# Optimization experiments

Hardware: AMD Instinct MI355X
Metric: run time of the kernel (lower is better)

Reference implementation:

```python
import jax, jax.numpy as jnp
import numpy as np

B = 16      # batch (num jagged sequences)
N = 1024    # max seq length (mask size n)
D = 512     # embedding_dim
H = 8       # num_heads
DA = 64     # attention_dim per head
DV = 64     # linear_hidden_dim per head
EPS = 1e-6


def setup_inputs() -> dict:
    key = jax.random.key(0)
    k0, k1, k2, k3 = jax.random.split(key, 4)
    lengths = 512 + 16 * np.arange(B)            # deterministic jagged lengths, all <= N
    offsets = np.concatenate([[0], np.cumsum(lengths)]).astype(np.int64)  # (B+1,)
    T = int(offsets[-1])                          # 10112 total tokens
    x = jax.random.normal(k0, (T, D), jnp.float32)
    uvqk = jax.random.normal(k1, (D, 2 * H * DV + 2 * H * DA), jnp.float32) * 0.02
    # torch Linear weight is (out_features, in_features) = (D, H*DV), xavier-uniform scale
    lim = float(np.sqrt(6.0 / (D + H * DV)))
    o_weight = jax.random.uniform(k2, (D, H * DV), jnp.float32, -lim, lim)
    o_bias = jax.random.uniform(k3, (D,), jnp.float32, -0.01, 0.01)
    invalid_attn_mask = jnp.tril(jnp.ones((N, N), jnp.float32))  # causal {0,1} mask
    return {
        "x": x,
        "x_offsets": jnp.asarray(offsets),
        "invalid_attn_mask": invalid_attn_mask,
        "uvqk": uvqk,
        "o_weight": o_weight,
        "o_bias": o_bias,
    }


def _layer_norm(x):
    # F.layer_norm over last dim, no elementwise affine
    m = jnp.mean(x, axis=-1, keepdims=True)
    v = jnp.mean(jnp.square(x - m), axis=-1, keepdims=True)
    return (x - m) / jnp.sqrt(v + EPS)


def _jagged_to_padded(values, offsets, n):
    # values: (T, C) -> (B, n, C), zero padded
    lengths = offsets[1:] - offsets[:-1]               # (B,)
    pos = jnp.arange(n)                                # (n,)
    idx = offsets[:-1, None] + pos[None, :]            # (B, n)
    valid = pos[None, :] < lengths[:, None]            # (B, n)
    idx = jnp.where(valid, idx, 0)
    return values[idx] * valid[..., None].astype(values.dtype)


def _dense_to_jagged(padded, offsets, T):
    # padded: (B, n, C) -> (T, C)
    tok = jnp.arange(T)
    b = jnp.searchsorted(offsets, tok, side="right") - 1   # batch id per token
    p = tok - offsets[b]                                   # position within sequence
    return padded[b, p]


def reference(x, x_offsets, invalid_attn_mask, uvqk, o_weight, o_bias):
    T = x.shape[0]
    n = invalid_attn_mask.shape[-1]
    normed_x = _layer_norm(x)                              # (T, D)
    mm = jax.nn.silu(normed_x @ uvqk)                      # (T, 2*H*DV + 2*H*DA)
    u, v, q, k = jnp.split(mm, [H * DV, 2 * H * DV, 2 * H * DV + H * DA], axis=1)
    pq = _jagged_to_padded(q, x_offsets, n).reshape(-1, n, H, DA)  # (B,n,H,DA)
    pk = _jagged_to_padded(k, x_offsets, n).reshape(-1, n, H, DA)
    pv = _jagged_to_padded(v, x_offsets, n).reshape(-1, n, H, DV)
    qk = jnp.einsum("bqhd,bkhd->bhqk", pq, pk)             # (B,H,n,n)
    qk = (jax.nn.silu(qk) / n) * invalid_attn_mask[None, None]
    attn = jnp.einsum("bhqk,bkhd->bqhd", qk, pv).reshape(-1, n, H * DV)
    attn_j = _dense_to_jagged(attn, x_offsets, T)          # (T, H*DV)
    o_input = u * _layer_norm(attn_j)
    return o_input @ o_weight.T + o_bias + x
```

## Files before the change

### kernel.cpp

```cpp
#include <hip/hip_runtime.h>
#include <hip/hip_bf16.h>
#include <math.h>

typedef short bf16x8 __attribute__((ext_vector_type(8)));
typedef float f32x4 __attribute__((ext_vector_type(4)));

#define MFMA16x16(a, b, c) __builtin_amdgcn_mfma_f32_16x16x32_bf16(a, b, c, 0, 0, 0)

__device__ __forceinline__ float silu_f(float v) { return v / (1.0f + __expf(-v)); }
__device__ __forceinline__ int swz128(int b) { return b ^ (((b >> 7) & 7) << 4); }

__device__ __forceinline__ unsigned short f2bf(float f) {
  union { float f; unsigned u; } x; x.f = f;
  unsigned r = x.u + 0x7fffu + ((x.u >> 16) & 1u);
  return (unsigned short)(r >> 16);
}
__device__ __forceinline__ float bf2f(unsigned short h) {
  union { unsigned u; float f; } x; x.u = ((unsigned)h) << 16;
  return x.f;
}

__device__ __forceinline__ void gload_lds16(const void* g, void* l) {
  __builtin_amdgcn_global_load_lds((__attribute__((address_space(1))) unsigned int*)g,
                                   (__attribute__((address_space(3))) unsigned int*)l,
                                   16, 0, 0);
}

__global__ void k_prep_offs(const int* __restrict__ raw, int* __restrict__ offs, int Bp1) {
  int t = threadIdx.x;
  bool is64 = (raw[3] == 0);
  if (t < Bp1) offs[t] = is64 ? raw[2 * t] : raw[t];
}

__global__ __launch_bounds__(256) void k_conv_uvqkT(const float* __restrict__ uvqk,
                                                    unsigned short* __restrict__ uvqkT) {
  __shared__ float tile[32][33];
  int n0 = blockIdx.x * 32, k0 = blockIdx.y * 32;
  int tx = threadIdx.x & 31;
  int ty = threadIdx.x >> 5;
#pragma unroll
  for (int i = 0; i < 4; ++i)
    tile[ty + 8 * i][tx] = uvqk[(size_t)(k0 + ty + 8 * i) * 2048 + n0 + tx];
  __syncthreads();
#pragma unroll
  for (int i = 0; i < 4; ++i) {
    int nn = ty + 8 * i;
    uvqkT[(size_t)(n0 + nn) * 512 + k0 + tx] = f2bf(tile[tx][nn]);
  }
}

__global__ __launch_bounds__(256) void k_conv_bf16(const float* __restrict__ in,
                                                   unsigned short* __restrict__ out, int n) {
  int i = blockIdx.x * 256 + threadIdx.x;
  if (i < n) out[i] = f2bf(in[i]);
}

__global__ __launch_bounds__(256) void k_ln_x(const float* __restrict__ x,
                                              unsigned short* __restrict__ normed, int T) {
  int lane = threadIdx.x & 63, wid = threadIdx.x >> 6;
  int row = blockIdx.x * 4 + wid;
  if (row >= T) return;
  const float4* xr = (const float4*)(x + (size_t)row * 512);
  float4 a = xr[lane * 2], b = xr[lane * 2 + 1];
  float s = a.x + a.y + a.z + a.w + b.x + b.y + b.z + b.w;
  float s2 = a.x * a.x + a.y * a.y + a.z * a.z + a.w * a.w +
             b.x * b.x + b.y * b.y + b.z * b.z + b.w * b.w;
#pragma unroll
  for (int m = 1; m < 64; m <<= 1) { s += __shfl_xor(s, m); s2 += __shfl_xor(s2, m); }
  float mean = s * (1.0f / 512.0f);
  float var = s2 * (1.0f / 512.0f) - mean * mean;
  float rstd = rsqrtf(var + 1e-6f);
  float v[8] = {a.x, a.y, a.z, a.w, b.x, b.y, b.z, b.w};
  unsigned short o[8];
#pragma unroll
  for (int j = 0; j < 8; ++j) o[j] = f2bf((v[j] - mean) * rstd);
  *(uint4*)(normed + (size_t)row * 512 + lane * 8) = *(uint4*)o;
}

__global__ __launch_bounds__(256) void k_ln_mul_u(const unsigned short* __restrict__ attnb,
                                                  const unsigned short* __restrict__ mm,
                                                  unsigned short* __restrict__ oin, int T) {
  int lane = threadIdx.x & 63, wid = threadIdx.x >> 6;
  int row = blockIdx.x * 4 + wid;
  if (row >= T) return;
  uint4 av = *(const uint4*)(attnb + (size_t)row * 512 + lane * 8);
  const unsigned short* ae = (const unsigned short*)&av;
  float v[8];
#pragma unroll
  for (int j = 0; j < 8; ++j) v[j] = bf2f(ae[j]);
  float s = 0.f, s2 = 0.f;
#pragma unroll
  for (int j = 0; j < 8; ++j) { s += v[j]; s2 += v[j] * v[j]; }
#pragma unroll
  for (int m = 1; m < 64; m <<= 1) { s += __shfl_xor(s, m); s2 += __shfl_xor(s2, m); }
  float mean = s * (1.0f / 512.0f);
  float var = s2 * (1.0f / 512.0f) - mean * mean;
  float rstd = rsqrtf(var + 1e-6f);
  uint4 ub = *(const uint4*)(mm + (size_t)row * 2048 + lane * 8);
  const unsigned short* us = (const unsigned short*)&ub;
  unsigned short o[8];
#pragma unroll
  for (int j = 0; j < 8; ++j) o[j] = f2bf((v[j] - mean) * rstd * bf2f(us[j]));
  *(uint4*)(oin + (size_t)row * 512 + lane * 8) = *(uint4*)o;
}

template <int MODE>
__global__ __launch_bounds__(256) void k_gemm_bt(const unsigned short* __restrict__ A,
                                                 const unsigned short* __restrict__ Bt,
                                                 void* __restrict__ Cout,
                                                 const float* __restrict__ bias,
                                                 const float* __restrict__ xres,
                                                 int M, int Nn, int K, int ntn) {
  __shared__ __align__(16) char lds[32768];
  char* ldsA = lds;
  char* ldsB = lds + 16384;
  int bid = blockIdx.x;
  int mt = bid / ntn, nt = bid - mt * ntn;
  int m0 = mt * 128, n0 = nt * 128;
  int tid = threadIdx.x, lane = tid & 63, wid = tid >> 6;
  int wm = wid >> 1, wn = wid & 1;
  int fr = lane & 15, fq = lane >> 4;
  f32x4 acc[4][4] = {};
  int nK = K >> 6;
  int lco = (lane & 7) * 16;
  int lrow8 = lane >> 3;
  for (int kt = 0; kt < nK; ++kt) {
    int k0 = kt << 6;
#pragma unroll
    for (int p = 0; p < 4; ++p) {
      int chunk = wid * 4 + p;
      int row = chunk * 8 + lrow8;
      int colb = lco ^ ((row & 7) << 4);
      int ar = m0 + row; if (ar >= M) ar = M - 1;
      gload_lds16((const char*)(A + (size_t)ar * K + k0) + colb, ldsA + chunk * 1024);
      gload_lds16((const char*)(Bt + (size_t)(n0 + row) * K + k0) + colb, ldsB + chunk * 1024);
    }
    __syncthreads();
    bf16x8 af[4][2], bfr[4][2];
#pragma unroll
    for (int mi = 0; mi < 4; ++mi) {
      int r = wm * 64 + mi * 16 + fr;
#pragma unroll
      for (int kk = 0; kk < 2; ++kk)
        af[mi][kk] = *(const bf16x8*)(ldsA + swz128(r * 128 + kk * 64 + fq * 16));
    }
#pragma unroll
    for (int ni = 0; ni < 4; ++ni) {
      int r = wn * 64 + ni * 16 + fr;
#pragma unroll
      for (int kk = 0; kk < 2; ++kk)
        bfr[ni][kk] = *(const bf16x8*)(ldsB + swz128(r * 128 + kk * 64 + fq * 16));
    }
#pragma unroll
    for (int mi = 0; mi < 4; ++mi)
#pragma unroll
      for (int ni = 0; ni < 4; ++ni) {
        acc[mi][ni] = MFMA16x16(af[mi][0], bfr[ni][0], acc[mi][ni]);
        acc[mi][ni] = MFMA16x16(af[mi][1], bfr[ni][1], acc[mi][ni]);
      }
    __syncthreads();
  }
#pragma unroll
  for (int mi = 0; mi < 4; ++mi) {
#pragma unroll
    for (int j = 0; j < 4; ++j) {
      int r = m0 + wm * 64 + mi * 16 + fq * 4 + j;
      if (r >= M) continue;
#pragma unroll
      for (int ni = 0; ni < 4; ++ni) {
        int c = n0 + wn * 64 + ni * 16 + fr;
        float v = acc[mi][ni][j];
        if (MODE == 0) {
          ((unsigned short*)Cout)[(size_t)r * Nn + c] = f2bf(silu_f(v));
        } else {
          ((float*)Cout)[(size_t)r * Nn + c] = v + bias[c] + xres[(size_t)r * 512 + c];
        }
      }
    }
  }
}

__global__ __launch_bounds__(256) void k_vT(const unsigned short* __restrict__ mm,
                                            const int* __restrict__ offs,
                                            unsigned short* __restrict__ vT) {
  int bh = blockIdx.x; int b = bh >> 3, h = bh & 7;
  int off = offs[b], len = offs[b + 1] - off;
  int lane = threadIdx.x & 63, w = threadIdx.x >> 6;
  const unsigned short* vp = mm + (size_t)off * 2048 + 512 + h * 64 + lane;
  unsigned short* vt = vT + ((size_t)bh * 64 + lane) * 1024;
  int nc = ((len + 63) & ~63) >> 3;
  for (int c = w; c < nc; c += 4) {
    int s8 = c << 3;
    unsigned short r[8];
#pragma unroll
    for (int j = 0; j < 8; ++j)
      r[j] = (s8 + j < len) ? vp[(size_t)(s8 + j) * 2048] : (unsigned short)0;
    *(uint4*)(vt + s8) = *(uint4*)r;
  }
}

__global__ __launch_bounds__(256) void k_attn2(const unsigned short* __restrict__ mm,
                                               const unsigned short* __restrict__ vT,
                                               const int* __restrict__ offs,
                                               unsigned short* __restrict__ attnb,
                                               float inv_n) {
  __shared__ __align__(16) char sP[16384];
  int bid = blockIdx.x;
  int orig = (bid & 7) * 128 + (bid >> 3);
  int bh = orig >> 3, grp = orig & 7;
  int b = bh >> 3, h = bh & 7;
  int off = offs[b], len = offs[b + 1] - off;
  int tid = threadIdx.x, lane = tid & 63, wid = tid >> 6;
  int qb = grp * 128 + wid * 32;
  if (qb >= len) return;
  int fr = lane & 15, fq = lane >> 4;
  const unsigned short* qp = mm + (size_t)off * 2048 + 1024 + h * 64;
  const unsigned short* kp = mm + (size_t)off * 2048 + 1536 + h * 64;
  const unsigned short* vtp = vT + (size_t)bh * 64 * 1024;
  bf16x8 aq[2][2];
#pragma unroll
  for (int mi = 0; mi < 2; ++mi) {
    int qr = qb + mi * 16 + fr; if (qr >= len) qr = len - 1;
#pragma unroll
    for (int kk = 0; kk < 2; ++kk)
      aq[mi][kk] = *(const bf16x8*)(qp + (size_t)qr * 2048 + kk * 32 + fq * 8);
  }
  f32x4 accO[2][4] = {};
  char* pw = sP + wid * 4096;
  int nkt = (qb >> 6) + 1;
  for (int kt = 0; kt < nkt; ++kt) {
    int s0 = kt << 6;
    bf16x8 kf[4][2];
#pragma unroll
    for (int ni = 0; ni < 4; ++ni)
#pragma unroll
      for (int kk = 0; kk < 2; ++kk)
        kf[ni][kk] = *(const bf16x8*)(kp + (size_t)(s0 + ni * 16 + fr) * 2048 + kk * 32 + fq * 8);
#pragma unroll
    for (int mi = 0; mi < 2; ++mi) {
      f32x4 sacc[4] = {};
#pragma unroll
      for (int ni = 0; ni < 4; ++ni) {
        sacc[ni] = MFMA16x16(aq[mi][0], kf[ni][0], sacc[ni]);
        sacc[ni] = MFMA16x16(aq[mi][1], kf[ni][1], sacc[ni]);
      }
#pragma unroll
      for (int ni = 0; ni < 4; ++ni)
#pragma unroll
        for (int j = 0; j < 4; ++j) {
          int pq = qb + mi * 16 + fq * 4 + j;
          int ps = s0 + ni * 16 + fr;
          float v = (ps <= pq) ? silu_f(sacc[ni][j]) * inv_n : 0.0f;
          *(unsigned short*)(pw + swz128((mi * 16 + fq * 4 + j) * 128 + (ni * 16 + fr) * 2)) =
              f2bf(v);
        }
    }
    bf16x8 vf[4][2];
#pragma unroll
    for (int nd = 0; nd < 4; ++nd)
#pragma unroll
      for (int kk = 0; kk < 2; ++kk)
        vf[nd][kk] = *(const bf16x8*)(vtp + (size_t)(nd * 16 + fr) * 1024 + s0 + kk * 32 + fq * 8);
#pragma unroll
    for (int mi = 0; mi < 2; ++mi) {
      bf16x8 pa0 = *(const bf16x8*)(pw + swz128((mi * 16 + fr) * 128 + fq * 16));
      bf16x8 pa1 = *(const bf16x8*)(pw + swz128((mi * 16 + fr) * 128 + 64 + fq * 16));
#pragma unroll
      for (int nd = 0; nd < 4; ++nd) {
        accO[mi][nd] = MFMA16x16(pa0, vf[nd][0], accO[mi][nd]);
        accO[mi][nd] = MFMA16x16(pa1, vf[nd][1], accO[mi][nd]);
      }
    }
  }
#pragma unroll
  for (int mi = 0; mi < 2; ++mi)
#pragma unroll
    for (int nd = 0; nd < 4; ++nd)
#pragma unroll
      for (int j = 0; j < 4; ++j) {
        int pq = qb + mi * 16 + fq * 4 + j;
        if (pq < len)
          attnb[(size_t)(off + pq) * 512 + h * 64 + nd * 16 + fr] = f2bf(accO[mi][nd][j]);
      }
}

extern "C" void kernel_launch(void* const* d_in, const int* in_sizes, int n_in,
                              void* d_out, int out_size, void* d_ws, size_t ws_size,
                              hipStream_t stream) {
  const float* x = (const float*)d_in[0];
  const int* xoff = (const int*)d_in[1];
  const float* uvqk = (const float*)d_in[3];
  const float* ow = (const float*)d_in[4];
  const float* obias = (const float*)d_in[5];

  const int D = 512;
  int T = in_sizes[0] / D;
  int B = in_sizes[1] - 1;
  int nm = 1;
  while ((long long)nm * nm < (long long)in_sizes[2]) nm <<= 1;

  char* w = (char*)d_ws;
  size_t p = 0;
  auto alloc = [&](size_t bytes) { size_t r = p; p += (bytes + 255) & ~(size_t)255; return r; };
  int* offs = (int*)(w + alloc(sizeof(int) * (size_t)(B + 1)));
  unsigned short* normed = (unsigned short*)(w + alloc((size_t)T * 512 * 2));
  unsigned short* mm = (unsigned short*)(w + alloc((size_t)T * 2048 * 2));
  unsigned short* attnb = (unsigned short*)(w + alloc((size_t)T * 512 * 2));
  unsigned short* oin = (unsigned short*)(w + alloc((size_t)T * 512 * 2));
  unsigned short* uvqkT = (unsigned short*)(w + alloc((size_t)2048 * 512 * 2));
  unsigned short* owb = (unsigned short*)(w + alloc((size_t)512 * 512 * 2));
  unsigned short* vT = (unsigned short*)(w + alloc((size_t)B * 8 * 64 * (size_t)nm * 2));

  k_prep_offs<<<1, 32, 0, stream>>>(xoff, offs, B + 1);
  k_conv_uvqkT<<<dim3(64, 16), 256, 0, stream>>>(uvqk, uvqkT);
  k_conv_bf16<<<1024, 256, 0, stream>>>(ow, owb, 512 * 512);
  k_ln_x<<<(T + 3) / 4, 256, 0, stream>>>(x, normed, T);
  int ntm = (T + 127) / 128;
  k_gemm_bt<0><<<ntm * 16, 256, 0, stream>>>(normed, uvqkT, (void*)mm, nullptr, nullptr,
                                             T, 2048, 512, 16);
  k_vT<<<B * 8, 256, 0, stream>>>(mm, offs, vT);
  k_attn2<<<(B * 8 * nm / 128), 256, 0, stream>>>(mm, vT, offs, attnb, 1.0f / (float)nm);
  k_ln_mul_u<<<(T + 3) / 4, 256, 0, stream>>>(attnb, mm, oin, T);
  k_gemm_bt<1><<<ntm * 4, 256, 0, stream>>>(oin, owb, d_out, obias, x, T, 512, 512, 4);
}
```

Measured before the change: 261.8 us.

## Schedule attention work by descending q-tile with compacted K buffer

A prep kernel builds a list of valid (batch, q-tile) work items ordered from longest causal range to shortest, and the attention kernel assigns one wave per (tile, head) from that list. Waves for q-tiles past the sequence end are no longer launched, and long tiles start first to balance the load. K is also copied into a contiguous per-head buffer so its loads are dense rather than strided by 2048, and the QK loop is restructured to reuse each K fragment across both M sub-tiles. The cost is an extra K copy pass, a serial single-thread tile build, and more workspace.

```diff
diff --git a/kernel.cpp b/kernel.cpp
--- a/kernel.cpp
+++ b/kernel.cpp
@@ -26,10 +26,23 @@
                                    16, 0, 0);
 }
 
-__global__ void k_prep_offs(const int* __restrict__ raw, int* __restrict__ offs, int Bp1) {
+__global__ void k_prep(const int* __restrict__ raw, int Bp1, int* __restrict__ offs,
+                       int* __restrict__ tiles, int qtmax) {
   int t = threadIdx.x;
   bool is64 = (raw[3] == 0);
   if (t < Bp1) offs[t] = is64 ? raw[2 * t] : raw[t];
+  __syncthreads();
+  if (t == 0) {
+    int B = Bp1 - 1;
+    int cnt = 0;
+    for (int qt = qtmax - 1; qt >= 0; --qt)
+      for (int b = 0; b < B; ++b) {
+        int len = offs[b + 1] - offs[b];
+        int nt = (len + 31) >> 5;
+        if (qt < nt) tiles[1 + cnt++] = (b << 16) | qt;
+      }
+    tiles[0] = cnt * 8;
+  }
 }
 
 __global__ __launch_bounds__(256) void k_conv_uvqkT(const float* __restrict__ uvqk,
@@ -180,16 +193,26 @@
   }
 }
 
-__global__ __launch_bounds__(256) void k_vT(const unsigned short* __restrict__ mm,
+__global__ __launch_bounds__(256) void k_kv(const unsigned short* __restrict__ mm,
                                             const int* __restrict__ offs,
-                                            unsigned short* __restrict__ vT) {
+                                            unsigned short* __restrict__ kC,
+                                            unsigned short* __restrict__ vT, int ns) {
   int bh = blockIdx.x; int b = bh >> 3, h = bh & 7;
-  int off = offs[b], len = offs[b + 1] - off;
-  int lane = threadIdx.x & 63, w = threadIdx.x >> 6;
+  int off = offs[b], len = offs[b + 1] - offs[b];
+  int tid = threadIdx.x;
+  int npad = (len + 63) & ~63;
+  const unsigned short* kp = mm + (size_t)off * 2048 + 1536 + h * 64;
+  unsigned short* kc = kC + (size_t)bh * ns * 64;
+  for (int i = tid; i < npad * 8; i += 256) {
+    int row = i >> 3, c8 = (i & 7) * 8;
+    uint4 v = {0u, 0u, 0u, 0u};
+    if (row < len) v = *(const uint4*)(kp + (size_t)row * 2048 + c8);
+    *(uint4*)(kc + row * 64 + c8) = v;
+  }
+  int lane = tid & 63, w = tid >> 6;
   const unsigned short* vp = mm + (size_t)off * 2048 + 512 + h * 64 + lane;
-  unsigned short* vt = vT + ((size_t)bh * 64 + lane) * 1024;
-  int nc = ((len + 63) & ~63) >> 3;
-  for (int c = w; c < nc; c += 4) {
+  unsigned short* vt = vT + ((size_t)bh * 64 + lane) * ns;
+  for (int c = w; c < (npad >> 3); c += 4) {
     int s8 = c << 3;
     unsigned short r[8];
 #pragma unroll
@@ -199,24 +222,27 @@
   }
 }
 
-__global__ __launch_bounds__(256) void k_attn2(const unsigned short* __restrict__ mm,
+__global__ __launch_bounds__(256) void k_attn3(const unsigned short* __restrict__ mm,
+                                               const unsigned short* __restrict__ kC,
                                                const unsigned short* __restrict__ vT,
                                                const int* __restrict__ offs,
+                                               const int* __restrict__ tiles,
                                                unsigned short* __restrict__ attnb,
-                                               float inv_n) {
+                                               float inv_n, int ns) {
   __shared__ __align__(16) char sP[16384];
-  int bid = blockIdx.x;
-  int orig = (bid & 7) * 128 + (bid >> 3);
-  int bh = orig >> 3, grp = orig & 7;
-  int b = bh >> 3, h = bh & 7;
-  int off = offs[b], len = offs[b + 1] - off;
   int tid = threadIdx.x, lane = tid & 63, wid = tid >> 6;
-  int qb = grp * 128 + wid * 32;
-  if (qb >= len) return;
+  int w = blockIdx.x * 4 + wid;
+  if (w >= tiles[0]) return;
+  int e = tiles[1 + (w >> 3)];
+  int h = w & 7;
+  int b = e >> 16, qt = e & 0xffff;
+  int bh = b * 8 + h;
+  int off = offs[b], len = offs[b + 1] - offs[b];
+  int qb = qt * 32;
   int fr = lane & 15, fq = lane >> 4;
   const unsigned short* qp = mm + (size_t)off * 2048 + 1024 + h * 64;
-  const unsigned short* kp = mm + (size_t)off * 2048 + 1536 + h * 64;
-  const unsigned short* vtp = vT + (size_t)bh * 64 * 1024;
+  const unsigned short* kcp = kC + (size_t)bh * ns * 64;
+  const unsigned short* vtp = vT + (size_t)bh * 64 * ns;
   bf16x8 aq[2][2];
 #pragma unroll
   for (int mi = 0; mi < 2; ++mi) {
@@ -230,47 +256,49 @@
   int nkt = (qb >> 6) + 1;
   for (int kt = 0; kt < nkt; ++kt) {
     int s0 = kt << 6;
-    bf16x8 kf[4][2];
-#pragma unroll
-    for (int ni = 0; ni < 4; ++ni)
+    f32x4 sacc[2][4] = {};
+#pragma unroll
+    for (int ni = 0; ni < 4; ++ni) {
+      const unsigned short* kr = kcp + (size_t)(s0 + ni * 16 + fr) * 64 + fq * 8;
+      bf16x8 k0 = *(const bf16x8*)kr;
+      bf16x8 k1 = *(const bf16x8*)(kr + 32);
+#pragma unroll
+      for (int mi = 0; mi < 2; ++mi) {
+        sacc[mi][ni] = MFMA16x16(aq[mi][0], k0, sacc[mi][ni]);
+        sacc[mi][ni] = MFMA16x16(aq[mi][1], k1, sacc[mi][ni]);
+      }
+    }
+    bf16x8 vf[4][2];
+#pragma unroll
+    for (int nd = 0; nd < 4; ++nd)
 #pragma unroll
       for (int kk = 0; kk < 2; ++kk)
-        kf[ni][kk] = *(const bf16x8*)(kp + (size_t)(s0 + ni * 16 + fr) * 2048 + kk * 32 + fq * 8);
-#pragma unroll
-    for (int mi = 0; mi < 2; ++mi) {
-      f32x4 sacc[4] = {};
-#pragma unroll
-      for (int ni = 0; ni < 4; ++ni) {
-        sacc[ni] = MFMA16x16(aq[mi][0], kf[ni][0], sacc[ni]);
-        sacc[ni] = MFMA16x16(aq[mi][1], kf[ni][1], sacc[ni]);
-      }
+        vf[nd][kk] = *(const bf16x8*)(vtp + (size_t)(nd * 16 + fr) * ns + s0 + kk * 32 + fq * 8);
+#pragma unroll
+    for (int mi = 0; mi < 2; ++mi)
 #pragma unroll
       for (int ni = 0; ni < 4; ++ni)
 #pragma unroll
         for (int j = 0; j < 4; ++j) {
           int pq = qb + mi * 16 + fq * 4 + j;
           int ps = s0 + ni * 16 + fr;
-          float v = (ps <= pq) ? silu_f(sacc[ni][j]) * inv_n : 0.0f;
+          float v = (ps <= pq) ? silu_f(sacc[mi][ni][j]) * inv_n : 0.0f;
           *(unsigned short*)(pw + swz128((mi * 16 + fq * 4 + j) * 128 + (ni * 16 + fr) * 2)) =
               f2bf(v);
         }
-    }
-    bf16x8 vf[4][2];
+    bf16x8 pa[2][2];
+#pragma unroll
+    for (int mi = 0; mi < 2; ++mi) {
+      pa[mi][0] = *(const bf16x8*)(pw + swz128((mi * 16 + fr) * 128 + fq * 16));
+      pa[mi][1] = *(const bf16x8*)(pw + swz128((mi * 16 + fr) * 128 + 64 + fq * 16));
+    }
 #pragma unroll
     for (int nd = 0; nd < 4; ++nd)
 #pragma unroll
-      for (int kk = 0; kk < 2; ++kk)
-        vf[nd][kk] = *(const bf16x8*)(vtp + (size_t)(nd * 16 + fr) * 1024 + s0 + kk * 32 + fq * 8);
-#pragma unroll
-    for (int mi = 0; mi < 2; ++mi) {
-      bf16x8 pa0 = *(const bf16x8*)(pw + swz128((mi * 16 + fr) * 128 + fq * 16));
-      bf16x8 pa1 = *(const bf16x8*)(pw + swz128((mi * 16 + fr) * 128 + 64 + fq * 16));
-#pragma unroll
-      for (int nd = 0; nd < 4; ++nd) {
-        accO[mi][nd] = MFMA16x16(pa0, vf[nd][0], accO[mi][nd]);
-        accO[mi][nd] = MFMA16x16(pa1, vf[nd][1], accO[mi][nd]);
-      }
-    }
+      for (int mi = 0; mi < 2; ++mi) {
+        accO[mi][nd] = MFMA16x16(pa[mi][0], vf[nd][0], accO[mi][nd]);
+        accO[mi][nd] = MFMA16x16(pa[mi][1], vf[nd][1], accO[mi][nd]);
+      }
   }
 #pragma unroll
   for (int mi = 0; mi < 2; ++mi)
@@ -298,11 +326,13 @@
   int B = in_sizes[1] - 1;
   int nm = 1;
   while ((long long)nm * nm < (long long)in_sizes[2]) nm <<= 1;
+  int qtmax = nm / 32;
 
   char* w = (char*)d_ws;
   size_t p = 0;
   auto alloc = [&](size_t bytes) { size_t r = p; p += (bytes + 255) & ~(size_t)255; return r; };
   int* offs = (int*)(w + alloc(sizeof(int) * (size_t)(B + 1)));
+  int* tiles = (int*)(w + alloc(sizeof(int) * (size_t)(1 + B * qtmax)));
   unsigned short* normed = (unsigned short*)(w + alloc((size_t)T * 512 * 2));
   unsigned short* mm = (unsigned short*)(w + alloc((size_t)T * 2048 * 2));
   unsigned short* attnb = (unsigned short*)(w + alloc((size_t)T * 512 * 2));
@@ -310,16 +340,19 @@
   unsigned short* uvqkT = (unsigned short*)(w + alloc((size_t)2048 * 512 * 2));
   unsigned short* owb = (unsigned short*)(w + alloc((size_t)512 * 512 * 2));
   unsigned short* vT = (unsigned short*)(w + alloc((size_t)B * 8 * 64 * (size_t)nm * 2));
-
-  k_prep_offs<<<1, 32, 0, stream>>>(xoff, offs, B + 1);
+  unsigned short* kC = (unsigned short*)(w + alloc((size_t)B * 8 * (size_t)nm * 64 * 2));
+
+  k_prep<<<1, 256, 0, stream>>>(xoff, B + 1, offs, tiles, qtmax);
   k_conv_uvqkT<<<dim3(64, 16), 256, 0, stream>>>(uvqk, uvqkT);
   k_conv_bf16<<<1024, 256, 0, stream>>>(ow, owb, 512 * 512);
   k_ln_x<<<(T + 3) / 4, 256, 0, stream>>>(x, normed, T);
   int ntm = (T + 127) / 128;
   k_gemm_bt<0><<<ntm * 16, 256, 0, stream>>>(normed, uvqkT, (void*)mm, nullptr, nullptr,
                                              T, 2048, 512, 16);
-  k_vT<<<B * 8, 256, 0, stream>>>(mm, offs, vT);
-  k_attn2<<<(B * 8 * nm / 128), 256, 0, stream>>>(mm, vT, offs, attnb, 1.0f / (float)nm);
+  k_kv<<<B * 8, 256, 0, stream>>>(mm, offs, kC, vT, nm);
+  int maxw = B * qtmax * 8;
+  k_attn3<<<(maxw + 3) / 4, 256, 0, stream>>>(mm, kC, vT, offs, tiles, attnb,
+                                              1.0f / (float)nm, nm);
   k_ln_mul_u<<<(T + 3) / 4, 256, 0, stream>>>(attnb, mm, oin, T);
   k_gemm_bt<1><<<ntm * 4, 256, 0, stream>>>(oin, owb, d_out, obias, x, T, 512, 512, 4);
 }
```

New measurement: 293.7 us. +12.2%, slower.
